# Optimization experiments

Measured on AMD Instinct MI355X. Metric: run time of the kernel, lower is better.

The kernel has to match this reference:

```python
import jax, jax.numpy as jnp
import numpy as np

U = 50  # lstm units

def lstm_seq(x, Wx, Wh, b):
    # x: [B,S,D] -> h: [B,S,U], Keras LSTMCell gate order i,f,g,o
    B = x.shape[0]
    xz = jnp.einsum('bsd,dk->bsk', x, Wx) + b  # [B,S,4U]
    def step(carry, zt):
        h, c = carry
        z = zt + h @ Wh
        i, f, g, o = jnp.split(z, 4, axis=-1)
        c = jax.nn.sigmoid(f) * c + jax.nn.sigmoid(i) * jnp.tanh(g)
        h = jax.nn.sigmoid(o) * jnp.tanh(c)
        return (h, c), h
    init = (jnp.zeros((B, U), x.dtype), jnp.zeros((B, U), x.dtype))
    _, hs = jax.lax.scan(step, init, jnp.swapaxes(xz, 0, 1))
    return jnp.swapaxes(hs, 0, 1)

def bilstm(x, fWx, fWh, fb, bWx, bWh, bb):
    # Keras RNN(go_backwards=True) does NOT re-reverse outputs; concat as-is.
    fw = lstm_seq(x, fWx, fWh, fb)
    bw = lstm_seq(x[:, ::-1, :], bWx, bWh, bb)
    return jnp.concatenate([fw, bw], axis=-1)

def local_inference(x1e, m1, x2e, m2):
    # Literal translation: inputs are batch-first [B,S,D]; the TF code transposes
    # to [S,B,D] and batch-matmuls over the leading (seq) axis, so attention is
    # over the batch index at each timestep. A[s,i,j] = x1e[i,s]. x2e[j,s]
    A = jnp.einsum('isd,jsd->sij', x1e, x2e)
    m1t = m1.T  # [S,B]
    m2t = m2.T
    w2 = jnp.exp(A - jnp.max(A, axis=2, keepdims=True)) * m2t[:, None, :]
    alpha = w2 / (jnp.sum(w2, axis=-1, keepdims=True) + 1e-8)
    x1_dual = jnp.einsum('sij,jsd->isd', alpha, x2e)  # [B,S,D]
    A1 = A - jnp.max(A, axis=1, keepdims=True)
    w1 = jnp.exp(jnp.swapaxes(A1, 1, 2)) * m1t[:, None, :]
    beta = w1 / (jnp.sum(w1, axis=-1, keepdims=True) + 1e-8)
    x2_dual = jnp.einsum('sji,isd->jsd', beta, x1e)  # [B,S,D]
    return x1_dual, x2_dual

def esim_forward(x1, x2, emb, b1f_Wx, b1f_Wh, b1f_b, b1b_Wx, b1b_Wh, b1b_b,
                 dense_W, dense_b, b2f_Wx, b2f_Wh, b2f_b, b2b_Wx, b2b_Wh, b2b_b,
                 dense1_W, dense1_b, out_W, out_b):
    m1 = (x1 != 0).astype(jnp.float32)
    m2 = (x2 != 0).astype(jnp.float32)
    e1 = emb[x1] * m1[..., None]
    e2 = emb[x2] * m2[..., None]
    enc1 = bilstm(e1, b1f_Wx, b1f_Wh, b1f_b, b1b_Wx, b1b_Wh, b1b_b) * m1[..., None]
    enc2 = bilstm(e2, b1f_Wx, b1f_Wh, b1f_b, b1b_Wx, b1b_Wh, b1b_b) * m2[..., None]
    d1, d2 = local_inference(enc1, m1, enc2, m2)
    match1 = jnp.concatenate([enc1, d1, enc1 * d1, enc1 - d1], axis=2)
    match2 = jnp.concatenate([enc2, d2, enc2 * d2, enc2 - d2], axis=2)
    map1 = jax.nn.relu(match1 @ dense_W + dense_b)
    map2 = jax.nn.relu(match2 @ dense_W + dense_b)
    cmp1 = bilstm(map1, b2f_Wx, b2f_Wh, b2f_b, b2b_Wx, b2b_Wh, b2b_b)
    cmp2 = bilstm(map2, b2f_Wx, b2f_Wh, b2f_b, b2b_Wx, b2b_Wh, b2b_b)
    c1m = cmp1 * m1[..., None]
    c2m = cmp2 * m2[..., None]
    p1_sum = jnp.sum(c1m, axis=1) / jnp.sum(m1, axis=1)[:, None]
    p1_max = jnp.max(c1m, axis=1)
    p2_sum = jnp.sum(c2m, axis=1) / jnp.sum(m2, axis=1)[:, None]
    p2_max = jnp.max(c2m, axis=1)
    logit = jnp.concatenate([p1_sum, p1_max, p2_sum, p2_max], axis=1)
    logit = jnp.tanh(logit @ dense1_W + dense1_b)
    logit = logit @ out_W + out_b
    return jax.nn.softmax(logit, axis=-1)

def setup_inputs() -> dict:
    key = jax.random.key(0)
    ks = jax.random.split(key, 24)
    B, S, V, E = 128, 512, 20000, 50
    def w(k, shape, s=0.05):
        return jax.random.normal(k, shape, dtype=jnp.float32) * s
    return {
        'x1': jax.random.randint(ks[0], (B, S), 0, V, dtype=jnp.int32),
        'x2': jax.random.randint(ks[1], (B, S), 0, V, dtype=jnp.int32),
        'emb': jax.random.uniform(ks[2], (V, E), jnp.float32, -0.05, 0.05),
        'b1f_Wx': w(ks[3], (E, 4 * U)), 'b1f_Wh': w(ks[4], (U, 4 * U)), 'b1f_b': w(ks[5], (4 * U,)),
        'b1b_Wx': w(ks[6], (E, 4 * U)), 'b1b_Wh': w(ks[7], (U, 4 * U)), 'b1b_b': w(ks[8], (4 * U,)),
        'dense_W': w(ks[9], (400, 100), 0.02), 'dense_b': jnp.zeros((100,), jnp.float32),
        'b2f_Wx': w(ks[10], (100, 4 * U)), 'b2f_Wh': w(ks[11], (U, 4 * U)), 'b2f_b': w(ks[12], (4 * U,)),
        'b2b_Wx': w(ks[13], (100, 4 * U)), 'b2b_Wh': w(ks[14], (U, 4 * U)), 'b2b_b': w(ks[15], (4 * U,)),
        'dense1_W': w(ks[16], (400, 100), 0.02), 'dense1_b': jnp.zeros((100,), jnp.float32),
        'out_W': w(ks[17], (100, 2), 0.02), 'out_b': jnp.zeros((2,), jnp.float32),
    }

def reference(x1, x2, emb, b1f_Wx, b1f_Wh, b1f_b, b1b_Wx, b1b_Wh, b1b_b,
              dense_W, dense_b, b2f_Wx, b2f_Wh, b2f_b, b2b_Wx, b2b_Wh, b2b_b,
              dense1_W, dense1_b, out_W, out_b):
    return esim_forward(x1, x2, emb, b1f_Wx, b1f_Wh, b1f_b, b1b_Wx, b1b_Wh, b1b_b,
                        dense_W, dense_b, b2f_Wx, b2f_Wh, b2f_b, b2b_Wx, b2b_Wh, b2b_b,
                        dense1_W, dense1_b, out_W, out_b)
```

## Files before the change

kernel.cpp:

```cpp
#include <hip/hip_runtime.h>

#define TOKN 65536
#define SQ 512
#define BB 128
#define DD 100
#define APAD 132

typedef unsigned short bf16t;
typedef __attribute__((ext_vector_type(8))) short bf16x8;
typedef __attribute__((ext_vector_type(4))) float floatx4;

__device__ __forceinline__ float bf2f(bf16t v) {
  unsigned u = ((unsigned)v) << 16;
  return __uint_as_float(u);
}
__device__ __forceinline__ bf16t f2bf(float x) {
  unsigned u = __float_as_uint(x);
  unsigned r = u + 0x7FFFu + ((u >> 16) & 1u);
  return (bf16t)(r >> 16);
}
__device__ __forceinline__ float2 ldpair(const float* p) { return *(const float2*)p; }
__device__ __forceinline__ float2 ldpair(const bf16t* p) {
  unsigned u = *(const unsigned*)p;
  float2 r;
  r.x = __uint_as_float(u << 16);
  r.y = __uint_as_float(u & 0xFFFF0000u);
  return r;
}

__device__ __forceinline__ float sigm(float x) { return 1.f / (1.f + __expf(-x)); }
__device__ __forceinline__ float tanhx(float x) { return 1.f - 2.f / (1.f + __expf(2.f * x)); }

__global__ __launch_bounds__(256) void embed_kernel(
    const int* __restrict__ x1, const int* __restrict__ x2,
    const float* __restrict__ emb,
    bf16t* __restrict__ e1, bf16t* __restrict__ e2,
    float* __restrict__ m1, float* __restrict__ m2) {
  const int which = blockIdx.y;
  const int* __restrict__ x = which ? x2 : x1;
  bf16t* __restrict__ e = which ? e2 : e1;
  float* __restrict__ m = which ? m2 : m1;
  int idx = blockIdx.x * 256 + threadIdx.x;
  int t = idx >> 6, d = idx & 63;
  int tok = x[t];
  float mk = (tok != 0) ? 1.f : 0.f;
  float v = (d < 50) ? emb[tok * 50 + d] * mk : 0.f;
  e[idx] = f2bf(v);
  if (d == 0) m[t] = mk;
}

__global__ __launch_bounds__(256) void wprep_kernel(
    const float* __restrict__ w1f, const float* __restrict__ w1b,
    const float* __restrict__ w2f, const float* __restrict__ w2b,
    const float* __restrict__ dW,
    bf16t* __restrict__ w1T, bf16t* __restrict__ w2T, bf16t* __restrict__ wdT) {
  int idx = blockIdx.x * 256 + threadIdx.x;
  int sec = blockIdx.y;
  if (sec == 0) {
    if (idx >= 2 * 208 * 64) return;
    int d = idx / (208 * 64), r = idx % (208 * 64);
    int n = r >> 6, k = r & 63;
    const float* W = d ? w1b : w1f;
    float v = (n < 200 && k < 50) ? W[k * 200 + n] : 0.f;
    w1T[idx] = f2bf(v);
  } else if (sec == 1) {
    if (idx >= 2 * 208 * 128) return;
    int d = idx / (208 * 128), r = idx % (208 * 128);
    int n = r >> 7, k = r & 127;
    const float* W = d ? w2b : w2f;
    float v = (n < 200 && k < 100) ? W[k * 200 + n] : 0.f;
    w2T[idx] = f2bf(v);
  } else {
    if (idx >= 128 * 384) return;
    int n = idx / 384, kv = idx % 384;
    int reg = kv >> 7, kk = kv & 127;
    float v = 0.f;
    if (n < 100 && kk < 100) {
      if (reg == 0) v = dW[kk * 100 + n] + dW[(300 + kk) * 100 + n];
      else if (reg == 1) v = dW[(100 + kk) * 100 + n] - dW[(300 + kk) * 100 + n];
      else v = dW[(200 + kk) * 100 + n];
    }
    wdT[idx] = f2bf(v);
  }
}

template <int KP>
__global__ __launch_bounds__(256) void xz_mfma(
    const bf16t* __restrict__ A1, const bf16t* __restrict__ A2,
    const bf16t* __restrict__ WT,
    const float* __restrict__ bf_, const float* __restrict__ bb_,
    bf16t* __restrict__ out) {
  const int combo = blockIdx.y;
  const bf16t* __restrict__ A = (combo < 2) ? A1 : A2;
  const bf16t* __restrict__ W = WT + (size_t)(combo & 1) * 208 * KP;
  const float* __restrict__ bias = (combo & 1) ? bb_ : bf_;
  bf16t* __restrict__ O = out + (size_t)combo * TOKN * 200;
  const int tid = threadIdx.x;
  const int wave = tid >> 6, lane = tid & 63;
  const int m0 = blockIdx.x * 64 + wave * 16;
  const int l15 = lane & 15, quad = lane >> 4;
  floatx4 acc[13];
#pragma unroll
  for (int nt = 0; nt < 13; ++nt) acc[nt] = (floatx4){0.f, 0.f, 0.f, 0.f};
  const bf16t* __restrict__ arow = A + (size_t)(m0 + l15) * KP + quad * 8;
  const bf16t* __restrict__ wb = W + (size_t)l15 * KP + quad * 8;
#pragma unroll
  for (int ks = 0; ks < KP / 32; ++ks) {
    bf16x8 a = *(const bf16x8*)(arow + ks * 32);
#pragma unroll
    for (int nt = 0; nt < 13; ++nt) {
      bf16x8 b = *(const bf16x8*)(wb + (size_t)nt * 16 * KP + ks * 32);
      acc[nt] = __builtin_amdgcn_mfma_f32_16x16x32_bf16(a, b, acc[nt], 0, 0, 0);
    }
  }
  const int crow = m0 + quad * 4;
#pragma unroll
  for (int nt = 0; nt < 13; ++nt) {
    int n = nt * 16 + l15;
    if (n < 200) {
      float bn = bias[n];
#pragma unroll
      for (int r = 0; r < 4; ++r)
        O[(size_t)(crow + r) * 200 + n] = f2bf(acc[nt][r] + bn);
    }
  }
}

__global__ __launch_bounds__(256) void dense_mfma(
    const bf16t* __restrict__ enc1, const bf16t* __restrict__ enc2,
    const bf16t* __restrict__ d1b, const bf16t* __restrict__ d2b,
    const bf16t* __restrict__ wdT, const float* __restrict__ bias,
    bf16t* __restrict__ map1, bf16t* __restrict__ map2) {
  const int inp = blockIdx.y;
  const bf16t* __restrict__ E = inp ? enc2 : enc1;
  const bf16t* __restrict__ Db = inp ? d2b : d1b;
  bf16t* __restrict__ O = inp ? map2 : map1;
  const int tid = threadIdx.x;
  const int wave = tid >> 6, lane = tid & 63;
  const int m0 = blockIdx.x * 64 + wave * 16;
  const int l15 = lane & 15, quad = lane >> 4;
  floatx4 acc[8];
#pragma unroll
  for (int nt = 0; nt < 8; ++nt) acc[nt] = (floatx4){0.f, 0.f, 0.f, 0.f};
  const bf16t* __restrict__ erow = E + (size_t)(m0 + l15) * 128 + quad * 8;
  const bf16t* __restrict__ drow = Db + (size_t)(m0 + l15) * 128 + quad * 8;
  const bf16t* __restrict__ wb = wdT + (size_t)l15 * 384 + quad * 8;
#pragma unroll
  for (int ks = 0; ks < 4; ++ks) {
    bf16x8 ae = *(const bf16x8*)(erow + ks * 32);
    bf16x8 ad = *(const bf16x8*)(drow + ks * 32);
    bf16x8 aed;
#pragma unroll
    for (int q = 0; q < 8; ++q) {
      float pe = bf2f((bf16t)ae[q]);
      float pd = bf2f((bf16t)ad[q]);
      aed[q] = (short)f2bf(pe * pd);
    }
#pragma unroll
    for (int nt = 0; nt < 8; ++nt) {
      const bf16t* wn = wb + (size_t)nt * 16 * 384 + ks * 32;
      bf16x8 b0 = *(const bf16x8*)(wn);
      acc[nt] = __builtin_amdgcn_mfma_f32_16x16x32_bf16(ae, b0, acc[nt], 0, 0, 0);
      bf16x8 b1 = *(const bf16x8*)(wn + 128);
      acc[nt] = __builtin_amdgcn_mfma_f32_16x16x32_bf16(ad, b1, acc[nt], 0, 0, 0);
      bf16x8 b2 = *(const bf16x8*)(wn + 256);
      acc[nt] = __builtin_amdgcn_mfma_f32_16x16x32_bf16(aed, b2, acc[nt], 0, 0, 0);
    }
  }
  const int crow = m0 + quad * 4;
#pragma unroll
  for (int nt = 0; nt < 8; ++nt) {
    int n = nt * 16 + l15;
    float bn = (n < 100) ? bias[n] : 0.f;
#pragma unroll
    for (int r = 0; r < 4; ++r) {
      float v = (n < 100) ? fmaxf(acc[nt][r] + bn, 0.f) : 0.f;
      O[(size_t)(crow + r) * 128 + n] = f2bf(v);
    }
  }
}

__global__ __launch_bounds__(256) void lstm_scan(
    const bf16t* __restrict__ xz,
    const float* __restrict__ Whf, const float* __restrict__ Whb,
    bf16t* __restrict__ out1, bf16t* __restrict__ out2,
    const float* __restrict__ m1, const float* __restrict__ m2,
    int hasMask) {
  const int blk = blockIdx.x;
  const int scan = blk >> 7;
  const int b = blk & 127;
  const int inp = scan >> 1;
  const int dir = scan & 1;
  const float* __restrict__ Wh = dir ? Whb : Whf;
  const bf16t* __restrict__ xzs = xz + (size_t)scan * TOKN * 200 + (size_t)b * SQ * 200;
  bf16t* __restrict__ outRaw = (inp ? out2 : out1) + (size_t)b * SQ * 128;
  bf16t* __restrict__ outp = outRaw + dir * 50;
  const float* __restrict__ mk = (inp ? m2 : m1) + b * SQ;

  const int tid = threadIdx.x;
  const int lane = tid & 63;
  const int u = tid >> 2, g = tid & 3;
  const int col = g * 50 + u;
  __shared__ __align__(16) bf16t hb[2][64];

  float whc[50];
  if (tid < 200) {
#pragma unroll
    for (int k = 0; k < 50; ++k) whc[k] = Wh[k * 200 + col];
  }
  if (tid < 128) ((bf16t*)hb)[tid] = 0;
  float c = 0.f;
  float z0 = 0.f, z1 = 0.f;
  if (tid < 200) {
    z0 = bf2f(xzs[(size_t)(dir ? (SQ - 1) : 0) * 200 + col]);
    z1 = bf2f(xzs[(size_t)(dir ? (SQ - 2) : 1) * 200 + col]);
  }
  __syncthreads();
  for (int t = 0; t < SQ; ++t) {
    int tp = (t + 2 < SQ) ? (t + 2) : (SQ - 1);
    int rowp = dir ? (SQ - 1 - tp) : tp;
    float znext = 0.f;
    if (tid < 200) {
      znext = bf2f(xzs[(size_t)rowp * 200 + col]);
      const uint4* hp = (const uint4*)&hb[t & 1][0];
      uint4 q0 = hp[0], q1 = hp[1], q2 = hp[2];
      unsigned qL = *(const unsigned*)&hb[t & 1][48];
      float za = z0, zb = 0.f, zc = 0.f, zd = 0.f;
      unsigned dw[13] = {q0.x, q0.y, q0.z, q0.w, q1.x, q1.y, q1.z, q1.w,
                         q2.x, q2.y, q2.z, q2.w, qL};
#pragma unroll
      for (int p = 0; p < 13; ++p) {
        float h0 = __uint_as_float(dw[p] << 16);
        float h1 = __uint_as_float(dw[p] & 0xFFFF0000u);
        if (p & 1) {
          zc = fmaf(h0, whc[2 * p], zc);
          zd = fmaf(h1, whc[2 * p + 1], zd);
        } else {
          za = fmaf(h0, whc[2 * p], za);
          if (p < 12) zb = fmaf(h1, whc[2 * p + 1], zb);
        }
      }
      float z = (za + zb) + (zc + zd);
      float a = (g == 2) ? tanhx(z) : sigm(z);
      int base = lane & ~3;
      float ai = __shfl(a, base + 0);
      float af = __shfl(a, base + 1);
      float ag_ = __shfl(a, base + 2);
      float ao = __shfl(a, base + 3);
      if (g == 0) {
        c = af * c + ai * ag_;
        float hn = ao * tanhx(c);
        hb[(t + 1) & 1][u] = f2bf(hn);
        float mv = hasMask ? mk[t] : 1.f;
        outp[(size_t)t * 128 + u] = f2bf(hn * mv);
      }
    } else if (dir == 0 && tid < 214) {
      *(unsigned*)&outRaw[(size_t)t * 128 + 100 + 2 * (tid - 200)] = 0u;
    }
    __syncthreads();
    z0 = z1;
    z1 = znext;
  }
}

__global__ __launch_bounds__(256) void attn_kernel(
    const bf16t* __restrict__ enc1, const bf16t* __restrict__ enc2,
    const float* __restrict__ m1, const float* __restrict__ m2,
    bf16t* __restrict__ d1b, bf16t* __restrict__ d2b) {
  const int s = blockIdx.x;
  const int tid = threadIdx.x;
  __shared__ __align__(16) float E1[BB][DD];
  __shared__ __align__(16) float E2[BB + 1][DD];
  __shared__ __align__(16) float Ah[64][APAD];
  __shared__ float mk1[BB], mk2[BB];
  __shared__ float rden[64];

  for (int idx = tid; idx < BB * 50; idx += 256) {
    int i = idx / 50, dp = idx - i * 50;
    float2 v1 = ldpair(enc1 + ((size_t)i * SQ + s) * 128 + 2 * dp);
    E1[i][2 * dp] = v1.x;
    E1[i][2 * dp + 1] = v1.y;
    float2 v2 = ldpair(enc2 + ((size_t)i * SQ + s) * 128 + 2 * dp);
    E2[i][2 * dp] = v2.x;
    E2[i][2 * dp + 1] = v2.y;
  }
  if (tid < BB) {
    mk1[tid] = m1[tid * SQ + s];
    mk2[tid] = m2[tid * SQ + s];
  }
  __syncthreads();

  const int ti = tid >> 4, tjj = tid & 15;
  const int xj = tid & 127;
  const int xd0 = (tid >> 7) * 50;
  float N[50];
#pragma unroll
  for (int q = 0; q < 50; ++q) N[q] = 0.f;
  float Dacc = 0.f, M = -1e30f;

  for (int half = 0; half < 2; ++half) {
    const int r0 = half * 64;
    float acc[4][8];
#pragma unroll
    for (int ii = 0; ii < 4; ++ii)
#pragma unroll
      for (int jj = 0; jj < 8; ++jj) acc[ii][jj] = 0.f;
    for (int k = 0; k < DD; k += 4) {
      float4 a4[4], b4[8];
#pragma unroll
      for (int ii = 0; ii < 4; ++ii)
        a4[ii] = *(const float4*)&E1[r0 + 4 * ti + ii][k];
#pragma unroll
      for (int jj = 0; jj < 8; ++jj)
        b4[jj] = *(const float4*)&E2[tjj + 16 * jj][k];
#pragma unroll
      for (int ii = 0; ii < 4; ++ii)
#pragma unroll
        for (int jj = 0; jj < 8; ++jj)
          acc[ii][jj] += a4[ii].x * b4[jj].x + a4[ii].y * b4[jj].y +
                         a4[ii].z * b4[jj].z + a4[ii].w * b4[jj].w;
    }
#pragma unroll
    for (int ii = 0; ii < 4; ++ii)
#pragma unroll
      for (int jj = 0; jj < 8; ++jj)
        Ah[4 * ti + ii][tjj + 16 * jj] = acc[ii][jj];
    __syncthreads();

    {
      float lm = M;
      for (int i = 0; i < 64; ++i) lm = fmaxf(lm, Ah[i][xj]);
      float scale = __expf(M - lm);
      Dacc *= scale;
#pragma unroll
      for (int q = 0; q < 50; ++q) N[q] *= scale;
      for (int i = 0; i < 64; ++i) {
        float p = __expf(Ah[i][xj] - lm) * mk1[r0 + i];
        Dacc += p;
        const float2* e1p = (const float2*)&E1[r0 + i][xd0];
#pragma unroll
        for (int q = 0; q < 25; ++q) {
          float2 ev = e1p[q];
          N[2 * q] += p * ev.x;
          N[2 * q + 1] += p * ev.y;
        }
      }
      M = lm;
    }
    __syncthreads();

    {
      int row = tid >> 2, seg = tid & 3;
      float mx = -1e30f;
      for (int q = 0; q < 32; ++q) mx = fmaxf(mx, Ah[row][seg + 4 * q]);
      mx = fmaxf(mx, __shfl_xor(mx, 1));
      mx = fmaxf(mx, __shfl_xor(mx, 2));
      float sm = 0.f;
      for (int q = 0; q < 32; ++q) {
        int jc = seg + 4 * q;
        float p = __expf(Ah[row][jc] - mx) * mk2[jc];
        Ah[row][jc] = p;
        sm += p;
      }
      sm += __shfl_xor(sm, 1);
      sm += __shfl_xor(sm, 2);
      if (seg == 0) rden[row] = sm + 1e-8f;
    }
    __syncthreads();

    {
      float o[4][8];
#pragma unroll
      for (int ii = 0; ii < 4; ++ii)
#pragma unroll
        for (int jj = 0; jj < 8; ++jj) o[ii][jj] = 0.f;
      for (int jb = 0; jb < BB; ++jb) {
        float pv[4], ev[8];
#pragma unroll
        for (int ii = 0; ii < 4; ++ii) pv[ii] = Ah[4 * ti + ii][jb];
#pragma unroll
        for (int jj = 0; jj < 8; ++jj) ev[jj] = E2[jb][tjj + 16 * jj];
#pragma unroll
        for (int ii = 0; ii < 4; ++ii)
#pragma unroll
          for (int jj = 0; jj < 8; ++jj) o[ii][jj] += pv[ii] * ev[jj];
      }
#pragma unroll
      for (int ii = 0; ii < 4; ++ii) {
        int i = r0 + 4 * ti + ii;
        float inv = 1.f / rden[4 * ti + ii];
#pragma unroll
        for (int jj = 0; jj < 8; ++jj) {
          int d = tjj + 16 * jj;
          float val = (d < DD) ? o[ii][jj] * inv : 0.f;
          d1b[((size_t)i * SQ + s) * 128 + d] = f2bf(val);
        }
      }
    }
    __syncthreads();
  }
  float invD = 1.f / (Dacc + 1e-8f);
#pragma unroll
  for (int q = 0; q < 50; ++q)
    d2b[((size_t)xj * SQ + s) * 128 + xd0 + q] = f2bf(N[q] * invD);
  if (xd0 == 50) {
#pragma unroll
    for (int q = 0; q < 28; ++q)
      d2b[((size_t)xj * SQ + s) * 128 + 100 + q] = 0;
  }
}

__global__ __launch_bounds__(128) void pool_kernel(
    const bf16t* __restrict__ cmp1, const bf16t* __restrict__ cmp2,
    const float* __restrict__ m1, const float* __restrict__ m2,
    float* __restrict__ pooled) {
  int b = blockIdx.x & 127, inp = blockIdx.x >> 7;
  const bf16t* C = (inp ? cmp2 : cmp1) + (size_t)b * SQ * 128;
  const float* M = (inp ? m2 : m1) + b * SQ;
  int f = threadIdx.x;
  float ms = 0.f;
  for (int s = f; s < SQ; s += 128) ms += M[s];
  __shared__ float red[128];
  red[f] = ms;
  __syncthreads();
  for (int o = 64; o > 0; o >>= 1) {
    if (f < o) red[f] += red[f + o];
    __syncthreads();
  }
  float msum = red[0];
  if (f < 100) {
    float sm = 0.f, mx = -1e30f;
    for (int s = 0; s < SQ; ++s) {
      float v = bf2f(C[(size_t)s * 128 + f]) * M[s];
      sm += v;
      mx = fmaxf(mx, v);
    }
    pooled[b * 400 + inp * 200 + f] = sm / msum;
    pooled[b * 400 + inp * 200 + 100 + f] = mx;
  }
}

__global__ __launch_bounds__(128) void final_kernel(
    const float* __restrict__ pooled, const float* __restrict__ W1,
    const float* __restrict__ b1, const float* __restrict__ W2,
    const float* __restrict__ b2, float* __restrict__ out) {
  int b = blockIdx.x;
  int j = threadIdx.x;
  __shared__ float pr[400];
  __shared__ float h[100];
  for (int idx = j; idx < 400; idx += 128) pr[idx] = pooled[b * 400 + idx];
  __syncthreads();
  if (j < 100) {
    float a = b1[j];
    for (int k = 0; k < 400; ++k) a += pr[k] * W1[k * 100 + j];
    h[j] = tanhx(a);
  }
  __syncthreads();
  if (j == 0) {
    float l0 = b2[0], l1 = b2[1];
    for (int k = 0; k < 100; ++k) {
      l0 += h[k] * W2[k * 2];
      l1 += h[k] * W2[k * 2 + 1];
    }
    float mx = fmaxf(l0, l1);
    float e0 = __expf(l0 - mx), e1 = __expf(l1 - mx);
    float inv = 1.f / (e0 + e1);
    out[b * 2] = e0 * inv;
    out[b * 2 + 1] = e1 * inv;
  }
}

extern "C" void kernel_launch(void* const* d_in, const int* in_sizes, int n_in,
                              void* d_out, int out_size, void* d_ws, size_t ws_size,
                              hipStream_t stream) {
  const int* x1 = (const int*)d_in[0];
  const int* x2 = (const int*)d_in[1];
  const float* emb = (const float*)d_in[2];
  const float* b1f_Wx = (const float*)d_in[3];
  const float* b1f_Wh = (const float*)d_in[4];
  const float* b1f_b = (const float*)d_in[5];
  const float* b1b_Wx = (const float*)d_in[6];
  const float* b1b_Wh = (const float*)d_in[7];
  const float* b1b_b = (const float*)d_in[8];
  const float* dense_W = (const float*)d_in[9];
  const float* dense_b = (const float*)d_in[10];
  const float* b2f_Wx = (const float*)d_in[11];
  const float* b2f_Wh = (const float*)d_in[12];
  const float* b2f_b = (const float*)d_in[13];
  const float* b2b_Wx = (const float*)d_in[14];
  const float* b2b_Wh = (const float*)d_in[15];
  const float* b2b_b = (const float*)d_in[16];
  const float* dense1_W = (const float*)d_in[17];
  const float* dense1_b = (const float*)d_in[18];
  const float* out_W = (const float*)d_in[19];
  const float* out_b = (const float*)d_in[20];
  float* out = (float*)d_out;

  char* base = (char*)d_ws;
  bf16t* xz = (bf16t*)base;
  bf16t* d1b = (bf16t*)base;
  bf16t* d2b = d1b + (size_t)TOKN * 128;
  char* r1 = base + (size_t)4 * TOKN * 200 * 2;
  bf16t* enc1 = (bf16t*)r1;
  bf16t* enc2 = enc1 + (size_t)TOKN * 128;
  bf16t* e1b = (bf16t*)r1;
  bf16t* e2b = e1b + (size_t)TOKN * 64;
  char* r2 = r1 + (size_t)2 * TOKN * 128 * 2;
  bf16t* map1 = (bf16t*)r2;
  bf16t* map2 = map1 + (size_t)TOKN * 128;
  char* r3 = r2 + (size_t)2 * TOKN * 128 * 2;
  float* m1 = (float*)r3;
  float* m2 = m1 + TOKN;
  float* pooled = m2 + TOKN;
  bf16t* w1T = (bf16t*)(r3 + ((size_t)2 * TOKN + 128 * 400) * 4);
  bf16t* w2T = w1T + 2 * 208 * 64;
  bf16t* wdT = w2T + 2 * 208 * 128;
  bf16t* cmp1 = enc1;
  bf16t* cmp2 = enc2;
  (void)in_sizes; (void)n_in; (void)out_size; (void)ws_size;

  embed_kernel<<<dim3(TOKN * 64 / 256, 2), 256, 0, stream>>>(
      x1, x2, emb, e1b, e2b, m1, m2);
  wprep_kernel<<<dim3(208, 3), 256, 0, stream>>>(
      b1f_Wx, b1b_Wx, b2f_Wx, b2b_Wx, dense_W, w1T, w2T, wdT);
  xz_mfma<64><<<dim3(TOKN / 64, 4), 256, 0, stream>>>(
      e1b, e2b, w1T, b1f_b, b1b_b, xz);
  lstm_scan<<<512, 256, 0, stream>>>(xz, b1f_Wh, b1b_Wh, enc1, enc2, m1, m2, 1);
  attn_kernel<<<SQ, 256, 0, stream>>>(enc1, enc2, m1, m2, d1b, d2b);
  dense_mfma<<<dim3(TOKN / 64, 2), 256, 0, stream>>>(
      enc1, enc2, d1b, d2b, wdT, dense_b, map1, map2);
  xz_mfma<128><<<dim3(TOKN / 64, 4), 256, 0, stream>>>(
      map1, map2, w2T, b2f_b, b2b_b, xz);
  lstm_scan<<<512, 256, 0, stream>>>(xz, b2f_Wh, b2b_Wh, cmp1, cmp2, m1, m2, 0);
  pool_kernel<<<256, 128, 0, stream>>>(cmp1, cmp2, m1, m2, pooled);
  final_kernel<<<128, 128, 0, stream>>>(pooled, dense1_W, dense1_b, out_W, out_b, out);
}
```

Baseline: 1.248 ms.

## Use packed fp16 dot2 for LSTM recurrent matvec with prepacked weights

The recurrent weights are prepacked into fp16 pairs in the weight-prep kernel, and the hidden state is kept in fp16 in shared memory. The per-step h·Wh product then uses v_dot2 instructions, halving the FMA count and register footprint (25 packed registers instead of 50 floats). The change also trims the gate shuffles to the lane that needs them and requests two blocks per CU via launch bounds. It trades some precision (fp16 weights and h instead of fp32 weights and bf16 h) and adds a small extra prep pass.

```diff
diff --git a/kernel.cpp b/kernel.cpp
--- a/kernel.cpp
+++ b/kernel.cpp
@@ -9,6 +9,7 @@
 typedef unsigned short bf16t;
 typedef __attribute__((ext_vector_type(8))) short bf16x8;
 typedef __attribute__((ext_vector_type(4))) float floatx4;
+typedef __attribute__((ext_vector_type(2))) _Float16 half2t;
 
 __device__ __forceinline__ float bf2f(bf16t v) {
   unsigned u = ((unsigned)v) << 16;
@@ -27,9 +28,20 @@
   r.y = __uint_as_float(u & 0xFFFF0000u);
   return r;
 }
+__device__ __forceinline__ half2t u2h2(unsigned u) {
+  union { unsigned u; half2t h; } x; x.u = u; return x.h;
+}
 
 __device__ __forceinline__ float sigm(float x) { return 1.f / (1.f + __expf(-x)); }
 __device__ __forceinline__ float tanhx(float x) { return 1.f - 2.f / (1.f + __expf(2.f * x)); }
+
+#if __has_builtin(__builtin_amdgcn_fdot2)
+#define DOT2(hu, wu, acc) acc = __builtin_amdgcn_fdot2(u2h2(hu), u2h2(wu), acc, false);
+#else
+#define DOT2(hu, wu, acc) { half2t hh = u2h2(hu), ww = u2h2(wu); \
+  acc = fmaf((float)hh[0], (float)ww[0], acc); \
+  acc = fmaf((float)hh[1], (float)ww[1], acc); }
+#endif
 
 __global__ __launch_bounds__(256) void embed_kernel(
     const int* __restrict__ x1, const int* __restrict__ x2,
@@ -53,7 +65,10 @@
     const float* __restrict__ w1f, const float* __restrict__ w1b,
     const float* __restrict__ w2f, const float* __restrict__ w2b,
     const float* __restrict__ dW,
-    bf16t* __restrict__ w1T, bf16t* __restrict__ w2T, bf16t* __restrict__ wdT) {
+    const float* __restrict__ h1f, const float* __restrict__ h1b,
+    const float* __restrict__ h2f, const float* __restrict__ h2b,
+    bf16t* __restrict__ w1T, bf16t* __restrict__ w2T, bf16t* __restrict__ wdT,
+    unsigned* __restrict__ whP) {
   int idx = blockIdx.x * 256 + threadIdx.x;
   int sec = blockIdx.y;
   if (sec == 0) {
@@ -70,7 +85,7 @@
     const float* W = d ? w2b : w2f;
     float v = (n < 200 && k < 100) ? W[k * 200 + n] : 0.f;
     w2T[idx] = f2bf(v);
-  } else {
+  } else if (sec == 2) {
     if (idx >= 128 * 384) return;
     int n = idx / 384, kv = idx % 384;
     int reg = kv >> 7, kk = kv & 127;
@@ -81,6 +96,17 @@
       else v = dW[(200 + kk) * 100 + n];
     }
     wdT[idx] = f2bf(v);
+  } else {
+    if (idx >= 4 * 25 * 200) return;
+    int sd = idx / 5000, r = idx % 5000;
+    int k2 = r / 200, colx = r % 200;
+    const float* W = (sd == 0) ? h1f : (sd == 1) ? h1b : (sd == 2) ? h2f : h2b;
+    float v0 = W[(2 * k2) * 200 + colx];
+    float v1 = W[(2 * k2 + 1) * 200 + colx];
+    union { _Float16 h[2]; unsigned u; } p;
+    p.h[0] = (_Float16)v0;
+    p.h[1] = (_Float16)v1;
+    whP[idx] = p.u;
   }
 }
 
@@ -180,9 +206,9 @@
   }
 }
 
-__global__ __launch_bounds__(256) void lstm_scan(
+__global__ __launch_bounds__(256, 2) void lstm_scan(
     const bf16t* __restrict__ xz,
-    const float* __restrict__ Whf, const float* __restrict__ Whb,
+    const unsigned* __restrict__ whPL,
     bf16t* __restrict__ out1, bf16t* __restrict__ out2,
     const float* __restrict__ m1, const float* __restrict__ m2,
     int hasMask) {
@@ -191,7 +217,6 @@
   const int b = blk & 127;
   const int inp = scan >> 1;
   const int dir = scan & 1;
-  const float* __restrict__ Wh = dir ? Whb : Whf;
   const bf16t* __restrict__ xzs = xz + (size_t)scan * TOKN * 200 + (size_t)b * SQ * 200;
   bf16t* __restrict__ outRaw = (inp ? out2 : out1) + (size_t)b * SQ * 128;
   bf16t* __restrict__ outp = outRaw + dir * 50;
@@ -201,14 +226,17 @@
   const int lane = tid & 63;
   const int u = tid >> 2, g = tid & 3;
   const int col = g * 50 + u;
-  __shared__ __align__(16) bf16t hb[2][64];
-
-  float whc[50];
-  if (tid < 200) {
-#pragma unroll
-    for (int k = 0; k < 50; ++k) whc[k] = Wh[k * 200 + col];
-  }
-  if (tid < 128) ((bf16t*)hb)[tid] = 0;
+  __shared__ __align__(16) unsigned hbuf[2][32];
+
+  const unsigned* __restrict__ wsrc = whPL + dir * 5000;
+  const int colc = (tid < 200) ? col : 0;
+  unsigned wreg[25];
+#pragma unroll
+  for (int k2 = 0; k2 < 25; ++k2) wreg[k2] = wsrc[k2 * 200 + colc];
+#pragma unroll
+  for (int k2 = 0; k2 < 25; ++k2) asm volatile("" : "+v"(wreg[k2]));
+
+  if (tid < 64) ((unsigned*)hbuf)[tid] = 0;
   float c = 0.f;
   float z0 = 0.f, z1 = 0.f;
   if (tid < 200) {
@@ -222,35 +250,33 @@
     float znext = 0.f;
     if (tid < 200) {
       znext = bf2f(xzs[(size_t)rowp * 200 + col]);
-      const uint4* hp = (const uint4*)&hb[t & 1][0];
-      uint4 q0 = hp[0], q1 = hp[1], q2 = hp[2];
-      unsigned qL = *(const unsigned*)&hb[t & 1][48];
+      const uint4* hp = (const uint4*)&hbuf[t & 1][0];
+      uint4 q0 = hp[0], q1 = hp[1], q2 = hp[2], q3 = hp[3], q4 = hp[4], q5 = hp[5];
+      unsigned qL = hbuf[t & 1][24];
       float za = z0, zb = 0.f, zc = 0.f, zd = 0.f;
-      unsigned dw[13] = {q0.x, q0.y, q0.z, q0.w, q1.x, q1.y, q1.z, q1.w,
-                         q2.x, q2.y, q2.z, q2.w, qL};
-#pragma unroll
-      for (int p = 0; p < 13; ++p) {
-        float h0 = __uint_as_float(dw[p] << 16);
-        float h1 = __uint_as_float(dw[p] & 0xFFFF0000u);
-        if (p & 1) {
-          zc = fmaf(h0, whc[2 * p], zc);
-          zd = fmaf(h1, whc[2 * p + 1], zd);
-        } else {
-          za = fmaf(h0, whc[2 * p], za);
-          if (p < 12) zb = fmaf(h1, whc[2 * p + 1], zb);
-        }
-      }
+      DOT2(q0.x, wreg[0], za)  DOT2(q0.y, wreg[1], zb)
+      DOT2(q0.z, wreg[2], zc)  DOT2(q0.w, wreg[3], zd)
+      DOT2(q1.x, wreg[4], za)  DOT2(q1.y, wreg[5], zb)
+      DOT2(q1.z, wreg[6], zc)  DOT2(q1.w, wreg[7], zd)
+      DOT2(q2.x, wreg[8], za)  DOT2(q2.y, wreg[9], zb)
+      DOT2(q2.z, wreg[10], zc) DOT2(q2.w, wreg[11], zd)
+      DOT2(q3.x, wreg[12], za) DOT2(q3.y, wreg[13], zb)
+      DOT2(q3.z, wreg[14], zc) DOT2(q3.w, wreg[15], zd)
+      DOT2(q4.x, wreg[16], za) DOT2(q4.y, wreg[17], zb)
+      DOT2(q4.z, wreg[18], zc) DOT2(q4.w, wreg[19], zd)
+      DOT2(q5.x, wreg[20], za) DOT2(q5.y, wreg[21], zb)
+      DOT2(q5.z, wreg[22], zc) DOT2(q5.w, wreg[23], zd)
+      DOT2(qL,   wreg[24], za)
       float z = (za + zb) + (zc + zd);
       float a = (g == 2) ? tanhx(z) : sigm(z);
       int base = lane & ~3;
-      float ai = __shfl(a, base + 0);
-      float af = __shfl(a, base + 1);
-      float ag_ = __shfl(a, base + 2);
-      float ao = __shfl(a, base + 3);
       if (g == 0) {
-        c = af * c + ai * ag_;
+        float af = __shfl(a, base + 1);
+        float ag_ = __shfl(a, base + 2);
+        float ao = __shfl(a, base + 3);
+        c = af * c + a * ag_;
         float hn = ao * tanhx(c);
-        hb[(t + 1) & 1][u] = f2bf(hn);
+        ((_Float16*)&hbuf[(t + 1) & 1][0])[u] = (_Float16)hn;
         float mv = hasMask ? mk[t] : 1.f;
         outp[(size_t)t * 128 + u] = f2bf(hn * mv);
       }
@@ -515,23 +541,25 @@
   bf16t* w1T = (bf16t*)(r3 + ((size_t)2 * TOKN + 128 * 400) * 4);
   bf16t* w2T = w1T + 2 * 208 * 64;
   bf16t* wdT = w2T + 2 * 208 * 128;
+  unsigned* whP = (unsigned*)(wdT + 128 * 384);
   bf16t* cmp1 = enc1;
   bf16t* cmp2 = enc2;
   (void)in_sizes; (void)n_in; (void)out_size; (void)ws_size;
 
   embed_kernel<<<dim3(TOKN * 64 / 256, 2), 256, 0, stream>>>(
       x1, x2, emb, e1b, e2b, m1, m2);
-  wprep_kernel<<<dim3(208, 3), 256, 0, stream>>>(
-      b1f_Wx, b1b_Wx, b2f_Wx, b2b_Wx, dense_W, w1T, w2T, wdT);
+  wprep_kernel<<<dim3(208, 4), 256, 0, stream>>>(
+      b1f_Wx, b1b_Wx, b2f_Wx, b2b_Wx, dense_W,
+      b1f_Wh, b1b_Wh, b2f_Wh, b2b_Wh, w1T, w2T, wdT, whP);
   xz_mfma<64><<<dim3(TOKN / 64, 4), 256, 0, stream>>>(
       e1b, e2b, w1T, b1f_b, b1b_b, xz);
-  lstm_scan<<<512, 256, 0, stream>>>(xz, b1f_Wh, b1b_Wh, enc1, enc2, m1, m2, 1);
+  lstm_scan<<<512, 256, 0, stream>>>(xz, whP, enc1, enc2, m1, m2, 1);
   attn_kernel<<<SQ, 256, 0, stream>>>(enc1, enc2, m1, m2, d1b, d2b);
   dense_mfma<<<dim3(TOKN / 64, 2), 256, 0, stream>>>(
       enc1, enc2, d1b, d2b, wdT, dense_b, map1, map2);
   xz_mfma<128><<<dim3(TOKN / 64, 4), 256, 0, stream>>>(
       map1, map2, w2T, b2f_b, b2b_b, xz);
-  lstm_scan<<<512, 256, 0, stream>>>(xz, b2f_Wh, b2b_Wh, cmp1, cmp2, m1, m2, 0);
+  lstm_scan<<<512, 256, 0, stream>>>(xz, whP + 2 * 5000, cmp1, cmp2, m1, m2, 0);
   pool_kernel<<<256, 128, 0, stream>>>(cmp1, cmp2, m1, m2, pooled);
   final_kernel<<<128, 128, 0, stream>>>(pooled, dense1_W, dense1_b, out_W, out_b, out);
 }
```

Measured after the change: 1.243 ms. No clear change (-0.4%).
